# Kernel optimization log

Measured on AMD Instinct MI355X. Metric: run time of the kernel, lower is better.

## Reference

```python
import jax, jax.numpy as jnp
import numpy as np

NUM_HEADS = 16


def rotary_pos_emb(x):
    # x: [b, h, s, d] with interleaved rotary pairs (d even)
    d, s = x.shape[-1], x.shape[-2]
    ts = jnp.arange(0, d, 2, dtype=jnp.float32)
    inv_freqs = 10000.0 ** (-ts / d)                      # [d/2]
    grid = jnp.arange(s, dtype=jnp.float32)[:, None] * inv_freqs[None, :]  # [s, d/2]
    sin = jnp.repeat(jnp.sin(grid), 2, axis=-1)           # [s, d]
    cos = jnp.repeat(jnp.cos(grid), 2, axis=-1)           # [s, d]
    x1, x2 = x[..., ::2], x[..., 1::2]
    xs = jnp.stack([-x2, x1], axis=-1).reshape(x.shape)   # rotate pairs
    return x * cos + xs * sin


def setup_inputs() -> dict:
    key = jax.random.key(0)
    ks = jax.random.split(key, 6)
    b, l, d = 2, 2048, 1024
    x = jax.random.normal(ks[0], (b, l, d), dtype=jnp.float32)
    # additive causal mask: 0 on/below diag, large negative above
    causal = jnp.tril(jnp.ones((l, l), dtype=bool))
    mask = jnp.where(causal, 0.0, -1e9).astype(jnp.float32)[None, None]  # [1,1,l,l]
    s = 0.01  # VarianceScaling(0.01)-ish small init
    Wq = jax.random.normal(ks[1], (d, d), dtype=jnp.float32) * s
    Wk = jax.random.normal(ks[2], (d, d), dtype=jnp.float32) * s
    Wv = jax.random.normal(ks[3], (d, d), dtype=jnp.float32) * s
    Wo = jax.random.normal(ks[4], (d, d), dtype=jnp.float32) * s
    return {"x": x, "mask": mask, "Wq": Wq, "Wk": Wk, "Wv": Wv, "Wo": Wo}


def reference(x, mask, Wq, Wk, Wv, Wo):
    b, l, d = x.shape
    h = NUM_HEADS
    k_sz = d // h
    split = lambda t: t.reshape(b, l, h, k_sz).transpose(0, 2, 1, 3)  # b h l k
    # NOTE: original scales q by 1/sqrt(model_dim) (not key_size), before RoPE
    q = split(x @ Wq / jnp.sqrt(jnp.float32(d)))
    q = rotary_pos_emb(q)
    k = rotary_pos_emb(split(x @ Wk))
    v = split(x @ Wv)
    logits = jnp.einsum('bhik,bhjk->bhij', q, k) + mask   # [b,h,l,l]
    a = jax.nn.softmax(logits, axis=-1)
    y = jnp.einsum('bhij,bhjv->bhiv', a, v)               # [b,h,l,k]
    y = y.transpose(0, 2, 1, 3).reshape(b, l, d)
    return y @ Wo
```

## Files before the change

kernel.cpp:

```cpp
#include <hip/hip_runtime.h>
#include <math.h>

#define L 2048
#define D 1024
#define H 16
#define KS 64
#define BBATCH 2

typedef float f32x4 __attribute__((ext_vector_type(4)));
typedef short s16x8 __attribute__((ext_vector_type(8)));

__device__ __forceinline__ ushort f2bf(float f) {
    union { float f; unsigned u; } v; v.f = f;
    unsigned lsb = (v.u >> 16) & 1u;
    v.u += 0x7fffu + lsb;
    return (ushort)(v.u >> 16);
}

__device__ __forceinline__ unsigned fbits(float f) {
    union { float f; unsigned u; } v; v.f = f; return v.u;
}

__device__ __forceinline__ void gl_lds16(const ushort* g, ushort* l) {
    __builtin_amdgcn_global_load_lds(
        (const __attribute__((address_space(1))) unsigned int*)g,
        (__attribute__((address_space(3))) unsigned int*)l, 16, 0, 0);
}

__global__ __launch_bounds__(256)
void prep(const float* __restrict__ x,
          const float* __restrict__ W0, const float* __restrict__ W1,
          const float* __restrict__ W2, const float* __restrict__ W3,
          ushort* __restrict__ xb, ushort* __restrict__ Wt,
          float2* __restrict__ tab)
{
    __shared__ float T[32][33];
    const int bid = blockIdx.x;
    const int tid = threadIdx.x;
    if (bid < 4096) {
        const int i = bid * 1024 + tid * 4;
        const float4 v = *(const float4*)&x[i];
        ushort4 p = make_ushort4(f2bf(v.x), f2bf(v.y), f2bf(v.z), f2bf(v.w));
        *(ushort4*)&xb[i] = p;
    } else if (bid < 8192) {
        const int t = bid - 4096;
        const int z = t >> 10;
        const float* W = (z == 0) ? W0 : (z == 1) ? W1 : (z == 2) ? W2 : W3;
        ushort* out = Wt + (size_t)z * D * D;
        const int r0 = ((t >> 5) & 31) * 32, c0 = (t & 31) * 32;
        const int tr = tid >> 3, tc = (tid & 7) * 4;
        const float4 v = *(const float4*)&W[(size_t)(r0 + tr) * D + c0 + tc];
        T[tr][tc + 0] = v.x; T[tr][tc + 1] = v.y;
        T[tr][tc + 2] = v.z; T[tr][tc + 3] = v.w;
        __syncthreads();
        ushort4 p = make_ushort4(f2bf(T[tc + 0][tr]), f2bf(T[tc + 1][tr]),
                                 f2bf(T[tc + 2][tr]), f2bf(T[tc + 3][tr]));
        *(ushort4*)&out[(size_t)(c0 + tr) * D + r0 + tc] = p;
    } else {
        const int idx = (bid - 8192) * 256 + tid;
        const int dd2 = idx >> 11, s = idx & 2047;
        const float inv = __expf(-(float)(2 * dd2) * (9.210340371976184f / 64.0f));
        float sn, cs;
        sincosf((float)s * inv, &sn, &cs);
        tab[idx] = make_float2(cs, sn);
    }
}

__global__ __launch_bounds__(256)
void qkv_gemm(const ushort* __restrict__ A, const ushort* __restrict__ B,
              const float2* __restrict__ tab,
              ushort* __restrict__ Qo, ushort* __restrict__ Ko,
              ushort* __restrict__ Vto)
{
    __shared__ __align__(16) ushort smem[18432];
    const int tid  = threadIdx.x;
    const int wv   = tid >> 6, lane = tid & 63;
    const int i16  = lane & 15, quad = lane >> 4;
    const int wr   = wv >> 1, wc = wv & 1;
    const int m0   = blockIdx.y * 128;
    const int n0   = blockIdx.x * 128;

    const int cA0 = wv * 64 + lane, cA1 = 256 + wv * 64 + lane;

    f32x4 acc[4][4];
    #pragma unroll
    for (int i = 0; i < 4; ++i)
        #pragma unroll
        for (int j = 0; j < 4; ++j) acc[i][j] = (f32x4){0.f, 0.f, 0.f, 0.f};

    {
        ushort* As = smem;
        ushort* Bs = smem + 4096;
        gl_lds16(A + (size_t)(m0 + (cA0 >> 2)) * D + (cA0 & 3) * 8, As + (size_t)(wv * 64) * 8);
        gl_lds16(A + (size_t)(m0 + (cA1 >> 2)) * D + (cA1 & 3) * 8, As + (size_t)(256 + wv * 64) * 8);
        gl_lds16(B + (size_t)(n0 + (cA0 >> 2)) * D + (cA0 & 3) * 8, Bs + (size_t)(wv * 64) * 8);
        gl_lds16(B + (size_t)(n0 + (cA1 >> 2)) * D + (cA1 & 3) * 8, Bs + (size_t)(256 + wv * 64) * 8);
    }
    __syncthreads();

    for (int it = 0; it < 32; ++it) {
        const int cur = it & 1;
        if (it + 1 < 32) {
            const int kn = (it + 1) * 32;
            ushort* As = smem + (cur ^ 1) * 8192;
            ushort* Bs = As + 4096;
            gl_lds16(A + (size_t)(m0 + (cA0 >> 2)) * D + kn + (cA0 & 3) * 8, As + (size_t)(wv * 64) * 8);
            gl_lds16(A + (size_t)(m0 + (cA1 >> 2)) * D + kn + (cA1 & 3) * 8, As + (size_t)(256 + wv * 64) * 8);
            gl_lds16(B + (size_t)(n0 + (cA0 >> 2)) * D + kn + (cA0 & 3) * 8, Bs + (size_t)(wv * 64) * 8);
            gl_lds16(B + (size_t)(n0 + (cA1 >> 2)) * D + kn + (cA1 & 3) * 8, Bs + (size_t)(256 + wv * 64) * 8);
        }
        const ushort* As = smem + cur * 8192;
        const ushort* Bs = As + 4096;
        s16x8 af[4], bf[4];
        #pragma unroll
        for (int mt = 0; mt < 4; ++mt)
            af[mt] = *(const s16x8*)&As[(wr * 64 + mt * 16 + i16) * 32 + quad * 8];
        #pragma unroll
        for (int nt = 0; nt < 4; ++nt)
            bf[nt] = *(const s16x8*)&Bs[(wc * 64 + nt * 16 + i16) * 32 + quad * 8];
        #pragma unroll
        for (int mt = 0; mt < 4; ++mt)
            #pragma unroll
            for (int nt = 0; nt < 4; ++nt)
                acc[mt][nt] = __builtin_amdgcn_mfma_f32_16x16x32_bf16(
                    af[mt], bf[nt], acc[mt][nt], 0, 0, 0);
        __syncthreads();
    }

    if (m0 < 2048) {
        const bool isQ = (m0 < 1024);
        ushort* out = isQ ? Qo : Ko;
        const int mb = isQ ? m0 : (m0 - 1024);
        #pragma unroll
        for (int mt = 0; mt < 4; ++mt)
            #pragma unroll
            for (int nt = 0; nt < 4; ++nt) {
                const int token = n0 + wc * 64 + nt * 16 + i16;
                const int b = token >> 11, s = token & 2047;
                const int dim = mb + wr * 64 + mt * 16 + quad * 4;
                const int hh = dim >> 6, dd = dim & 63;
                ushort4 p;
                #pragma unroll
                for (int pr = 0; pr < 2; ++pr) {
                    float e = acc[mt][nt][2 * pr];
                    float o = acc[mt][nt][2 * pr + 1];
                    if (isQ) { e *= 0.03125f; o *= 0.03125f; }
                    const float2 cssn = tab[(size_t)((dd >> 1) + pr) * 2048 + s];
                    const float ne = e * cssn.x - o * cssn.y;
                    const float no = o * cssn.x + e * cssn.y;
                    if (pr == 0) { p.x = f2bf(ne); p.y = f2bf(no); }
                    else         { p.z = f2bf(ne); p.w = f2bf(no); }
                }
                *(ushort4*)&out[((size_t)(b * H + hh) * L + s) * KS + dd] = p;
            }
    } else {
        ushort* T = smem + wv * 4608;
        const int vbase = (m0 - 2048) + wr * 64;
        const int tbase = n0 + wc * 64;
        #pragma unroll
        for (int mt = 0; mt < 4; ++mt)
            #pragma unroll
            for (int nt = 0; nt < 4; ++nt) {
                const int tl = nt * 16 + i16;
                #pragma unroll
                for (int r = 0; r < 4; ++r)
                    T[(mt * 16 + quad * 4 + r) * 72 + tl] = f2bf(acc[mt][nt][r]);
            }
        __builtin_amdgcn_s_waitcnt(0);
        const int tl0 = (lane & 7) * 8;
        #pragma unroll
        for (int c = 0; c < 8; ++c) {
            const int vl = c * 8 + (lane >> 3);
            const s16x8 val = *(const s16x8*)&T[vl * 72 + tl0];
            const int vdim = vbase + vl;
            const int hh = vdim >> 6, dd = vdim & 63;
            const int token0 = tbase + tl0;
            const int b = token0 >> 11, s0 = token0 & 2047;
            *(s16x8*)&Vto[((size_t)(b * H + hh) * KS + dd) * L + s0] = val;
        }
    }
}

__global__ __launch_bounds__(256)
void oproj_gemm(const ushort* __restrict__ A, const ushort* __restrict__ B,
                float* __restrict__ out)
{
    __shared__ __align__(16) ushort smem[12288];
    const int tid  = threadIdx.x;
    const int wv   = tid >> 6, lane = tid & 63;
    const int i16  = lane & 15, quad = lane >> 4;
    const int wr   = wv >> 1, wc = wv & 1;
    const int m0   = blockIdx.y * 128;
    const int n0   = blockIdx.x * 64;

    const int cA0 = wv * 64 + lane, cA1 = 256 + wv * 64 + lane;

    f32x4 acc[4][2];
    #pragma unroll
    for (int i = 0; i < 4; ++i)
        #pragma unroll
        for (int j = 0; j < 2; ++j) acc[i][j] = (f32x4){0.f, 0.f, 0.f, 0.f};

    {
        ushort* As = smem;
        ushort* Bs = smem + 4096;
        gl_lds16(A + (size_t)(m0 + (cA0 >> 2)) * D + (cA0 & 3) * 8, As + (size_t)(wv * 64) * 8);
        gl_lds16(A + (size_t)(m0 + (cA1 >> 2)) * D + (cA1 & 3) * 8, As + (size_t)(256 + wv * 64) * 8);
        gl_lds16(B + (size_t)(n0 + (cA0 >> 2)) * D + (cA0 & 3) * 8, Bs + (size_t)(wv * 64) * 8);
    }
    __syncthreads();

    for (int it = 0; it < 32; ++it) {
        const int cur = it & 1;
        if (it + 1 < 32) {
            const int kn = (it + 1) * 32;
            ushort* As = smem + (cur ^ 1) * 6144;
            ushort* Bs = As + 4096;
            gl_lds16(A + (size_t)(m0 + (cA0 >> 2)) * D + kn + (cA0 & 3) * 8, As + (size_t)(wv * 64) * 8);
            gl_lds16(A + (size_t)(m0 + (cA1 >> 2)) * D + kn + (cA1 & 3) * 8, As + (size_t)(256 + wv * 64) * 8);
            gl_lds16(B + (size_t)(n0 + (cA0 >> 2)) * D + kn + (cA0 & 3) * 8, Bs + (size_t)(wv * 64) * 8);
        }
        const ushort* As = smem + cur * 6144;
        const ushort* Bs = As + 4096;
        s16x8 af[4], bf[2];
        #pragma unroll
        for (int mt = 0; mt < 4; ++mt)
            af[mt] = *(const s16x8*)&As[(wr * 64 + mt * 16 + i16) * 32 + quad * 8];
        #pragma unroll
        for (int nt = 0; nt < 2; ++nt)
            bf[nt] = *(const s16x8*)&Bs[(wc * 32 + nt * 16 + i16) * 32 + quad * 8];
        #pragma unroll
        for (int mt = 0; mt < 4; ++mt)
            #pragma unroll
            for (int nt = 0; nt < 2; ++nt)
                acc[mt][nt] = __builtin_amdgcn_mfma_f32_16x16x32_bf16(
                    af[mt], bf[nt], acc[mt][nt], 0, 0, 0);
        __syncthreads();
    }

    #pragma unroll
    for (int mt = 0; mt < 4; ++mt)
        #pragma unroll
        for (int nt = 0; nt < 2; ++nt) {
            const int od = n0 + wc * 32 + nt * 16 + i16;
            const int tk = m0 + wr * 64 + mt * 16 + quad * 4;
            #pragma unroll
            for (int r = 0; r < 4; ++r)
                out[(size_t)(tk + r) * D + od] = acc[mt][nt][r];
        }
}

__global__ __launch_bounds__(512)
void attn_mfma(const ushort* __restrict__ Q, const ushort* __restrict__ K,
               const ushort* __restrict__ Vt, ushort* __restrict__ Yb)
{
    const int bh   = blockIdx.y;
    const int qa   = blockIdx.x;
    const int qb   = 31 - qa;
    const int tid  = threadIdx.x;
    const int wave = tid >> 6, lane = tid & 63;
    const int half = wave >> 2, wv4 = wave & 3;
    const int i16  = lane & 15, quad = lane >> 4;
    const int qt   = half ? qb : qa;
    const int r0   = qt * 64 + wv4 * 16;
    const int row  = r0 + i16;

    __shared__ ushort Ks[2][64 * 72];
    __shared__ ushort Vs[2][64 * 72];
    __shared__ ushort Ps[8][16 * 72];

    const ushort* Qb = Q  + (size_t)bh * L * KS;
    const ushort* Kb = K  + (size_t)bh * L * KS;
    const ushort* Vb = Vt + (size_t)bh * KS * L;

    const s16x8 qf0 = *(const s16x8*)(Qb + (size_t)row * KS + quad * 8);
    const s16x8 qf1 = *(const s16x8*)(Qb + (size_t)row * KS + 32 + quad * 8);

    const int sr = tid >> 3, sseg = (tid & 7) * 8;
    s16x8 kpre = *(const s16x8*)(Kb + (size_t)sr * KS + sseg);
    s16x8 vpre = *(const s16x8*)(Vb + (size_t)sr * L + sseg);
    *(s16x8*)&Ks[0][sr * 72 + sseg] = kpre;
    *(s16x8*)&Vs[0][sr * 72 + sseg] = vpre;
    __syncthreads();

    f32x4 O0 = {0.f,0.f,0.f,0.f}, O1 = O0, O2 = O0, O3 = O0;
    float psum = 0.0f;

    for (int jt = 0; jt <= qb; ++jt) {
        const int cur = jt & 1;
        const bool has_next = (jt < qb);

        if (has_next) {
            const int j0n = (jt + 1) * 64;
            kpre = *(const s16x8*)(Kb + (size_t)(j0n + sr) * KS + sseg);
            vpre = *(const s16x8*)(Vb + (size_t)sr * L + j0n + sseg);
        }

        if (jt <= qt) {
            const int j0 = jt * 64;
            const ushort* Ksb = &Ks[cur][0];
            const ushort* Vsb = &Vs[cur][0];
            f32x4 st[4];
            #pragma unroll
            for (int nt = 0; nt < 4; ++nt) {
                const s16x8 kf0 = *(const s16x8*)&Ksb[(nt * 16 + i16) * 72 + quad * 8];
                const s16x8 kf1 = *(const s16x8*)&Ksb[(nt * 16 + i16) * 72 + 32 + quad * 8];
                f32x4 c = {0.f,0.f,0.f,0.f};
                c = __builtin_amdgcn_mfma_f32_16x16x32_bf16(kf0, qf0, c, 0, 0, 0);
                c = __builtin_amdgcn_mfma_f32_16x16x32_bf16(kf1, qf1, c, 0, 0, 0);
                st[nt] = c;
            }
            if (jt == qt) {
                #pragma unroll
                for (int nt = 0; nt < 4; ++nt)
                    #pragma unroll
                    for (int rg = 0; rg < 4; ++rg) {
                        const int j = j0 + nt * 16 + quad * 4 + rg;
                        if (j > row) st[nt][rg] = -1e30f;
                    }
            }
            float pv[4][4];
            #pragma unroll
            for (int nt = 0; nt < 4; ++nt)
                #pragma unroll
                for (int rg = 0; rg < 4; ++rg) {
                    pv[nt][rg] = __expf(st[nt][rg]);
                    psum += pv[nt][rg];
                }
            ushort* P2 = &Ps[wave][0];
            #pragma unroll
            for (int nt = 0; nt < 4; ++nt) {
                uint2 pk;
                pk.x = __builtin_amdgcn_perm(fbits(pv[nt][1]), fbits(pv[nt][0]), 0x07060302u);
                pk.y = __builtin_amdgcn_perm(fbits(pv[nt][3]), fbits(pv[nt][2]), 0x07060302u);
                *(uint2*)(P2 + i16 * 72 + nt * 16 + quad * 4) = pk;
            }
            const s16x8 pf0 = *(const s16x8*)(P2 + i16 * 72 + quad * 8);
            const s16x8 pf1 = *(const s16x8*)(P2 + i16 * 72 + 32 + quad * 8);
            s16x8 v0, v1;
            v0 = *(const s16x8*)&Vsb[(0 * 16 + i16) * 72 + quad * 8];
            v1 = *(const s16x8*)&Vsb[(0 * 16 + i16) * 72 + 32 + quad * 8];
            O0 = __builtin_amdgcn_mfma_f32_16x16x32_bf16(v0, pf0, O0, 0, 0, 0);
            O0 = __builtin_amdgcn_mfma_f32_16x16x32_bf16(v1, pf1, O0, 0, 0, 0);
            v0 = *(const s16x8*)&Vsb[(1 * 16 + i16) * 72 + quad * 8];
            v1 = *(const s16x8*)&Vsb[(1 * 16 + i16) * 72 + 32 + quad * 8];
            O1 = __builtin_amdgcn_mfma_f32_16x16x32_bf16(v0, pf0, O1, 0, 0, 0);
            O1 = __builtin_amdgcn_mfma_f32_16x16x32_bf16(v1, pf1, O1, 0, 0, 0);
            v0 = *(const s16x8*)&Vsb[(2 * 16 + i16) * 72 + quad * 8];
            v1 = *(const s16x8*)&Vsb[(2 * 16 + i16) * 72 + 32 + quad * 8];
            O2 = __builtin_amdgcn_mfma_f32_16x16x32_bf16(v0, pf0, O2, 0, 0, 0);
            O2 = __builtin_amdgcn_mfma_f32_16x16x32_bf16(v1, pf1, O2, 0, 0, 0);
            v0 = *(const s16x8*)&Vsb[(3 * 16 + i16) * 72 + quad * 8];
            v1 = *(const s16x8*)&Vsb[(3 * 16 + i16) * 72 + 32 + quad * 8];
            O3 = __builtin_amdgcn_mfma_f32_16x16x32_bf16(v0, pf0, O3, 0, 0, 0);
            O3 = __builtin_amdgcn_mfma_f32_16x16x32_bf16(v1, pf1, O3, 0, 0, 0);
        }

        if (has_next) {
            *(s16x8*)&Ks[cur ^ 1][sr * 72 + sseg] = kpre;
            *(s16x8*)&Vs[cur ^ 1][sr * 72 + sseg] = vpre;
            __syncthreads();
        }
    }

    psum += __shfl_xor(psum, 16);
    psum += __shfl_xor(psum, 32);
    const float inv_l = __builtin_amdgcn_rcpf(psum);
    const int b = bh >> 4, hh = bh & 15;
    ushort* Yp = Yb + ((size_t)(b * L + row)) * D + hh * KS + quad * 4;
    f32x4 r;
    r = O0 * inv_l; *(ushort4*)(Yp +  0) = make_ushort4(f2bf(r[0]),f2bf(r[1]),f2bf(r[2]),f2bf(r[3]));
    r = O1 * inv_l; *(ushort4*)(Yp + 16) = make_ushort4(f2bf(r[0]),f2bf(r[1]),f2bf(r[2]),f2bf(r[3]));
    r = O2 * inv_l; *(ushort4*)(Yp + 32) = make_ushort4(f2bf(r[0]),f2bf(r[1]),f2bf(r[2]),f2bf(r[3]));
    r = O3 * inv_l; *(ushort4*)(Yp + 48) = make_ushort4(f2bf(r[0]),f2bf(r[1]),f2bf(r[2]),f2bf(r[3]));
}

extern "C" void kernel_launch(void* const* d_in, const int* in_sizes, int n_in,
                              void* d_out, int out_size, void* d_ws, size_t ws_size,
                              hipStream_t stream)
{
    const float* x  = (const float*)d_in[0];
    const float* Wq = (const float*)d_in[2];
    const float* Wk = (const float*)d_in[3];
    const float* Wv = (const float*)d_in[4];
    const float* Wo = (const float*)d_in[5];

    const size_t NTOK = (size_t)BBATCH * L;
    const size_t SZ   = NTOK * D;
    ushort* xb  = (ushort*)d_ws;
    ushort* Wt  = xb + SZ;
    ushort* Qb  = Wt + 4 * (size_t)D * D;
    ushort* Kb  = Qb + SZ;
    ushort* Vtb = Kb + SZ;
    ushort* Yb  = Vtb + SZ;
    float2* tab = (float2*)Yb;

    prep<<<dim3(8448), dim3(256), 0, stream>>>(x, Wq, Wk, Wv, Wo, xb, Wt, tab);

    qkv_gemm<<<dim3(32, 24), dim3(256), 0, stream>>>(Wt, xb, tab, Qb, Kb, Vtb);

    attn_mfma<<<dim3(16, 32), dim3(512), 0, stream>>>(Qb, Kb, Vtb, Yb);

    oproj_gemm<<<dim3(16, 32), dim3(256), 0, stream>>>(Yb, Wt + 3 * (size_t)D * D,
                                                       (float*)d_out);
}
```

Baseline: 193.7 us.

## Enlarge QKV GEMM tiles to 256x256 with a 4-stage swizzled LDS pipeline

Result: no change. 193.6 us (-0.1%).

```diff
diff --git a/kernel.cpp b/kernel.cpp
--- a/kernel.cpp
+++ b/kernel.cpp
@@ -66,84 +66,125 @@
     }
 }
 
-__global__ __launch_bounds__(256)
+__global__ __launch_bounds__(512, 2)
 void qkv_gemm(const ushort* __restrict__ A, const ushort* __restrict__ B,
               const float2* __restrict__ tab,
               ushort* __restrict__ Qo, ushort* __restrict__ Ko,
               ushort* __restrict__ Vto)
 {
-    __shared__ __align__(16) ushort smem[18432];
+    __shared__ __align__(16) ushort smem[65536];
     const int tid  = threadIdx.x;
     const int wv   = tid >> 6, lane = tid & 63;
     const int i16  = lane & 15, quad = lane >> 4;
-    const int wr   = wv >> 1, wc = wv & 1;
-    const int m0   = blockIdx.y * 128;
-    const int n0   = blockIdx.x * 128;
-
-    const int cA0 = wv * 64 + lane, cA1 = 256 + wv * 64 + lane;
-
-    f32x4 acc[4][4];
+    const int wr   = wv >> 2, wc = wv & 3;
+
+    int bid = blockIdx.y * 16 + blockIdx.x;
+    bid = (bid & 7) * 24 + (bid >> 3);
+    const int by = bid % 12, bx = bid / 12;
+    const int m0 = by * 256, n0 = bx * 256;
+
+    const int c0 = tid, c1 = tid + 512;
+    const size_t sA0 = (size_t)(m0 + (c0 >> 2)) * D + (((c0 & 3) * 8) ^ (((c0 >> 4) & 3) << 3));
+    const size_t sA1 = (size_t)(m0 + (c1 >> 2)) * D + (((c1 & 3) * 8) ^ (((c1 >> 4) & 3) << 3));
+    const size_t sB0 = (size_t)(n0 + (c0 >> 2)) * D + (((c0 & 3) * 8) ^ (((c0 >> 4) & 3) << 3));
+    const size_t sB1 = (size_t)(n0 + (c1 >> 2)) * D + (((c1 & 3) * 8) ^ (((c1 >> 4) & 3) << 3));
+    const int l0 = c0 * 8, l1 = c1 * 8;
+
+    f32x4 acc[8][4];
     #pragma unroll
-    for (int i = 0; i < 4; ++i)
+    for (int i = 0; i < 8; ++i)
         #pragma unroll
         for (int j = 0; j < 4; ++j) acc[i][j] = (f32x4){0.f, 0.f, 0.f, 0.f};
 
-    {
-        ushort* As = smem;
-        ushort* Bs = smem + 4096;
-        gl_lds16(A + (size_t)(m0 + (cA0 >> 2)) * D + (cA0 & 3) * 8, As + (size_t)(wv * 64) * 8);
-        gl_lds16(A + (size_t)(m0 + (cA1 >> 2)) * D + (cA1 & 3) * 8, As + (size_t)(256 + wv * 64) * 8);
-        gl_lds16(B + (size_t)(n0 + (cA0 >> 2)) * D + (cA0 & 3) * 8, Bs + (size_t)(wv * 64) * 8);
-        gl_lds16(B + (size_t)(n0 + (cA1 >> 2)) * D + (cA1 & 3) * 8, Bs + (size_t)(256 + wv * 64) * 8);
-    }
-    __syncthreads();
-
-    for (int it = 0; it < 32; ++it) {
-        const int cur = it & 1;
-        if (it + 1 < 32) {
-            const int kn = (it + 1) * 32;
-            ushort* As = smem + (cur ^ 1) * 8192;
-            ushort* Bs = As + 4096;
-            gl_lds16(A + (size_t)(m0 + (cA0 >> 2)) * D + kn + (cA0 & 3) * 8, As + (size_t)(wv * 64) * 8);
-            gl_lds16(A + (size_t)(m0 + (cA1 >> 2)) * D + kn + (cA1 & 3) * 8, As + (size_t)(256 + wv * 64) * 8);
-            gl_lds16(B + (size_t)(n0 + (cA0 >> 2)) * D + kn + (cA0 & 3) * 8, Bs + (size_t)(wv * 64) * 8);
-            gl_lds16(B + (size_t)(n0 + (cA1 >> 2)) * D + kn + (cA1 & 3) * 8, Bs + (size_t)(256 + wv * 64) * 8);
-        }
-        const ushort* As = smem + cur * 8192;
-        const ushort* Bs = As + 4096;
-        s16x8 af[4], bf[4];
-        #pragma unroll
-        for (int mt = 0; mt < 4; ++mt)
-            af[mt] = *(const s16x8*)&As[(wr * 64 + mt * 16 + i16) * 32 + quad * 8];
-        #pragma unroll
-        for (int nt = 0; nt < 4; ++nt)
-            bf[nt] = *(const s16x8*)&Bs[(wc * 64 + nt * 16 + i16) * 32 + quad * 8];
-        #pragma unroll
-        for (int mt = 0; mt < 4; ++mt)
-            #pragma unroll
-            for (int nt = 0; nt < 4; ++nt)
-                acc[mt][nt] = __builtin_amdgcn_mfma_f32_16x16x32_bf16(
-                    af[mt], bf[nt], acc[mt][nt], 0, 0, 0);
-        __syncthreads();
-    }
+#define STAGE_A(kt) do { ushort* As_ = smem + ((kt) & 3) * 16384;             \
+        gl_lds16(A + sA0 + (size_t)(kt) * 32, As_ + l0);                      \
+        gl_lds16(A + sA1 + (size_t)(kt) * 32, As_ + l1); } while (0)
+#define STAGE_B(kt) do { ushort* Bs_ = smem + ((kt) & 3) * 16384 + 8192;      \
+        gl_lds16(B + sB0 + (size_t)(kt) * 32, Bs_ + l0);                      \
+        gl_lds16(B + sB1 + (size_t)(kt) * 32, Bs_ + l1); } while (0)
+
+    STAGE_A(0); STAGE_B(0);
+    STAGE_A(1); STAGE_B(1);
+    STAGE_A(2); STAGE_B(2);
+    asm volatile("s_waitcnt vmcnt(8)" ::: "memory");
+    __builtin_amdgcn_s_barrier();
+
+    #pragma unroll 1
+    for (int kt = 0; kt < 32; ++kt) {
+        const ushort* As = smem + (kt & 3) * 16384;
+        const ushort* Bs = As + 8192;
+        s16x8 afr[4], bfr[4];
+
+        #pragma unroll
+        for (int mf = 0; mf < 4; ++mf) {
+            int ad = (wr * 128 + mf * 16 + i16) * 64 + quad * 16;
+            ad ^= ((ad >> 8) & 3) << 4;
+            afr[mf] = *(const s16x8*)((const char*)As + ad);
+        }
+        #pragma unroll
+        for (int nf = 0; nf < 4; ++nf) {
+            int ad = (wc * 64 + nf * 16 + i16) * 64 + quad * 16;
+            ad ^= ((ad >> 8) & 3) << 4;
+            bfr[nf] = *(const s16x8*)((const char*)Bs + ad);
+        }
+        if (kt < 29) STAGE_A(kt + 3);
+        __builtin_amdgcn_s_barrier();
+        asm volatile("s_waitcnt lgkmcnt(0)" ::: "memory");
+        __builtin_amdgcn_sched_barrier(0);
+        __builtin_amdgcn_s_setprio(1);
+        #pragma unroll
+        for (int mf = 0; mf < 4; ++mf)
+            #pragma unroll
+            for (int nf = 0; nf < 4; ++nf)
+                acc[mf][nf] = __builtin_amdgcn_mfma_f32_16x16x32_bf16(
+                    afr[mf], bfr[nf], acc[mf][nf], 0, 0, 0);
+        __builtin_amdgcn_s_setprio(0);
+        __builtin_amdgcn_s_barrier();
+
+        #pragma unroll
+        for (int mf = 0; mf < 4; ++mf) {
+            int ad = (wr * 128 + (mf + 4) * 16 + i16) * 64 + quad * 16;
+            ad ^= ((ad >> 8) & 3) << 4;
+            afr[mf] = *(const s16x8*)((const char*)As + ad);
+        }
+        if (kt < 29) STAGE_B(kt + 3);
+        __builtin_amdgcn_s_barrier();
+        asm volatile("s_waitcnt lgkmcnt(0)" ::: "memory");
+        __builtin_amdgcn_sched_barrier(0);
+        __builtin_amdgcn_s_setprio(1);
+        #pragma unroll
+        for (int mf = 0; mf < 4; ++mf)
+            #pragma unroll
+            for (int nf = 0; nf < 4; ++nf)
+                acc[mf + 4][nf] = __builtin_amdgcn_mfma_f32_16x16x32_bf16(
+                    afr[mf], bfr[nf], acc[mf + 4][nf], 0, 0, 0);
+        __builtin_amdgcn_s_setprio(0);
+
+        if (kt <= 28)      { asm volatile("s_waitcnt vmcnt(8)" ::: "memory"); }
+        else if (kt == 29) { asm volatile("s_waitcnt vmcnt(4)" ::: "memory"); }
+        else if (kt == 30) { asm volatile("s_waitcnt vmcnt(0)" ::: "memory"); }
+        __builtin_amdgcn_s_barrier();
+    }
+#undef STAGE_A
+#undef STAGE_B
 
     if (m0 < 2048) {
         const bool isQ = (m0 < 1024);
         ushort* out = isQ ? Qo : Ko;
-        const int mb = isQ ? m0 : (m0 - 1024);
-        #pragma unroll
-        for (int mt = 0; mt < 4; ++mt)
-            #pragma unroll
-            for (int nt = 0; nt < 4; ++nt) {
-                const int token = n0 + wc * 64 + nt * 16 + i16;
+        const int mb2 = isQ ? m0 : (m0 - 1024);
+        #pragma unroll
+        for (int mf = 0; mf < 8; ++mf)
+            #pragma unroll
+            for (int nf = 0; nf < 4; ++nf) {
+                const int token = n0 + wc * 64 + nf * 16 + i16;
                 const int b = token >> 11, s = token & 2047;
-                const int dim = mb + wr * 64 + mt * 16 + quad * 4;
+                const int dim = mb2 + wr * 128 + mf * 16 + quad * 4;
                 const int hh = dim >> 6, dd = dim & 63;
                 ushort4 p;
                 #pragma unroll
                 for (int pr = 0; pr < 2; ++pr) {
-                    float e = acc[mt][nt][2 * pr];
-                    float o = acc[mt][nt][2 * pr + 1];
+                    float e = acc[mf][nf][2 * pr];
+                    float o = acc[mf][nf][2 * pr + 1];
                     if (isQ) { e *= 0.03125f; o *= 0.03125f; }
                     const float2 cssn = tab[(size_t)((dd >> 1) + pr) * 2048 + s];
                     const float ne = e * cssn.x - o * cssn.y;
@@ -155,28 +196,32 @@
             }
     } else {
         ushort* T = smem + wv * 4608;
-        const int vbase = (m0 - 2048) + wr * 64;
         const int tbase = n0 + wc * 64;
         #pragma unroll
-        for (int mt = 0; mt < 4; ++mt)
-            #pragma unroll
-            for (int nt = 0; nt < 4; ++nt) {
-                const int tl = nt * 16 + i16;
+        for (int hh2 = 0; hh2 < 2; ++hh2) {
+            const int vbase = (m0 - 2048) + wr * 128 + hh2 * 64;
+            #pragma unroll
+            for (int mf = 0; mf < 4; ++mf)
                 #pragma unroll
-                for (int r = 0; r < 4; ++r)
-                    T[(mt * 16 + quad * 4 + r) * 72 + tl] = f2bf(acc[mt][nt][r]);
+                for (int nf = 0; nf < 4; ++nf) {
+                    #pragma unroll
+                    for (int r = 0; r < 4; ++r)
+                        T[(mf * 16 + quad * 4 + r) * 72 + nf * 16 + i16] =
+                            f2bf(acc[hh2 * 4 + mf][nf][r]);
+                }
+            __builtin_amdgcn_s_waitcnt(0);
+            const int tl0 = (lane & 7) * 8;
+            #pragma unroll
+            for (int c = 0; c < 8; ++c) {
+                const int vl = c * 8 + (lane >> 3);
+                const s16x8 val = *(const s16x8*)&T[vl * 72 + tl0];
+                const int vdim = vbase + vl;
+                const int hh = vdim >> 6, dd = vdim & 63;
+                const int token0 = tbase + tl0;
+                const int b = token0 >> 11, s0 = token0 & 2047;
+                *(s16x8*)&Vto[((size_t)(b * H + hh) * KS + dd) * L + s0] = val;
             }
-        __builtin_amdgcn_s_waitcnt(0);
-        const int tl0 = (lane & 7) * 8;
-        #pragma unroll
-        for (int c = 0; c < 8; ++c) {
-            const int vl = c * 8 + (lane >> 3);
-            const s16x8 val = *(const s16x8*)&T[vl * 72 + tl0];
-            const int vdim = vbase + vl;
-            const int hh = vdim >> 6, dd = vdim & 63;
-            const int token0 = tbase + tl0;
-            const int b = token0 >> 11, s0 = token0 & 2047;
-            *(s16x8*)&Vto[((size_t)(b * H + hh) * KS + dd) * L + s0] = val;
+            if (hh2 == 0) __builtin_amdgcn_s_waitcnt(0);
         }
     }
 }
@@ -397,7 +442,7 @@
 
     prep<<<dim3(8448), dim3(256), 0, stream>>>(x, Wq, Wk, Wv, Wo, xb, Wt, tab);
 
-    qkv_gemm<<<dim3(32, 24), dim3(256), 0, stream>>>(Wt, xb, tab, Qb, Kb, Vtb);
+    qkv_gemm<<<dim3(16, 12), dim3(512), 0, stream>>>(Wt, xb, tab, Qb, Kb, Vtb);
 
     attn_mfma<<<dim3(16, 32), dim3(512), 0, stream>>>(Qb, Kb, Vtb, Yb);
 
```
